# Kernel tuning notes

Measured on AMD Instinct MI355X. Metric: run time of the kernel, lower is better.

## Reference

```python
import jax, jax.numpy as jnp
import numpy as np

CLASS_NUM = 64
CENTROID_MARGIN = 1.4
EPS = 1e-6
N, D = 262144, 128


def setup_inputs() -> dict:
    key = jax.random.key(0)
    k1, k2 = jax.random.split(key)
    embeddings = jax.random.normal(k1, (N, D), dtype=jnp.float32)
    target = jax.random.randint(k2, (N,), 0, CLASS_NUM, dtype=jnp.int32)
    return {"embeddings": embeddings, "target": target}


def reference(embeddings, target):
    C = CLASS_NUM
    dt = embeddings.dtype
    # per-class sums and counts (equivalent to one-hot broadcast-multiply-sum in the original)
    counts = jax.ops.segment_sum(jnp.ones((embeddings.shape[0],), dtype=dt), target, num_segments=C)  # [C]
    sums = jax.ops.segment_sum(embeddings, target, num_segments=C)  # [C, D]
    class_centers = sums / (counts[:, None] + EPS)  # [C, D]
    # pairwise squared distances between centers
    diff = class_centers[:, None, :] - class_centers[None, :, :]  # [C, C, D]
    cc = jnp.sum(diff * diff, axis=2)  # [C, C]
    cc = jax.nn.relu(CENTROID_MARGIN - jnp.sqrt(cc + EPS)) ** 2
    cc = jnp.triu(cc, k=1).sum() / C * (C - 1) / 2
    # L2 distance of each embedding to its class center
    dist = embeddings - class_centers[target]  # [N, D]
    l2 = jnp.sum(dist * dist, axis=1).mean()
    return l2 + cc
```

## Files before the change

### kernel.cpp

```cpp
#include <hip/hip_runtime.h>

#define CLS 64
#define DIM 128
#define NROWS 262144
#define MARGIN 1.4f
#define EPSF 1e-6f
#define FIXSCALE 1048576.0f
#define INVFIX (1.0f / 1048576.0f)
#define NB 512

__global__ __launch_bounds__(512, 2) void phaseA(const float* __restrict__ emb,
                                                 const int* __restrict__ tgt,
                                                 float* __restrict__ psum,
                                                 int* __restrict__ pcnt,
                                                 float* __restrict__ psq,
                                                 int rowsPerBlock) {
    __shared__ int acc[CLS * DIM];
    __shared__ int cnt[CLS];
    __shared__ float red[8];
    const int tid = threadIdx.x;

    for (int i = tid; i < CLS * DIM; i += 512) acc[i] = 0;
    if (tid < CLS) cnt[tid] = 0;
    __syncthreads();

    const int dl = tid & 31;
    const int rl = tid >> 5;
    const int rowBase = blockIdx.x * rowsPerBlock;
    const int iters = rowsPerBlock >> 6;
    int r = rowBase + rl;

    const float4* __restrict__ embv = reinterpret_cast<const float4*>(emb);

    float4 v0 = embv[(size_t)(r)      * 32 + dl];
    float4 v1 = embv[(size_t)(r + 16) * 32 + dl];
    float4 v2 = embv[(size_t)(r + 32) * 32 + dl];
    float4 v3 = embv[(size_t)(r + 48) * 32 + dl];
    int c0 = tgt[r];
    int c1 = tgt[r + 16];
    int c2 = tgt[r + 32];
    int c3 = tgt[r + 48];

    float sq = 0.f;
    for (int it = 0; it < iters; ++it) {
        float4 x0 = v0, x1 = v1, x2 = v2, x3 = v3;
        int k0 = c0, k1 = c1, k2 = c2, k3 = c3;
        int rn = r + 64;
        if (it + 1 < iters) {
            v0 = embv[(size_t)(rn)      * 32 + dl];
            v1 = embv[(size_t)(rn + 16) * 32 + dl];
            v2 = embv[(size_t)(rn + 32) * 32 + dl];
            v3 = embv[(size_t)(rn + 48) * 32 + dl];
            c0 = tgt[rn];
            c1 = tgt[rn + 16];
            c2 = tgt[rn + 32];
            c3 = tgt[rn + 48];
        }
        r = rn;

        sq += x0.x * x0.x + x0.y * x0.y + x0.z * x0.z + x0.w * x0.w;
        sq += x1.x * x1.x + x1.y * x1.y + x1.z * x1.z + x1.w * x1.w;
        sq += x2.x * x2.x + x2.y * x2.y + x2.z * x2.z + x2.w * x2.w;
        sq += x3.x * x3.x + x3.y * x3.y + x3.z * x3.z + x3.w * x3.w;

        int* row0 = &acc[k0 * DIM];
        atomicAdd(&row0[dl],      __float2int_rn(x0.x * FIXSCALE));
        atomicAdd(&row0[32 + dl], __float2int_rn(x0.y * FIXSCALE));
        atomicAdd(&row0[64 + dl], __float2int_rn(x0.z * FIXSCALE));
        atomicAdd(&row0[96 + dl], __float2int_rn(x0.w * FIXSCALE));
        int* row1 = &acc[k1 * DIM];
        atomicAdd(&row1[dl],      __float2int_rn(x1.x * FIXSCALE));
        atomicAdd(&row1[32 + dl], __float2int_rn(x1.y * FIXSCALE));
        atomicAdd(&row1[64 + dl], __float2int_rn(x1.z * FIXSCALE));
        atomicAdd(&row1[96 + dl], __float2int_rn(x1.w * FIXSCALE));
        int* row2 = &acc[k2 * DIM];
        atomicAdd(&row2[dl],      __float2int_rn(x2.x * FIXSCALE));
        atomicAdd(&row2[32 + dl], __float2int_rn(x2.y * FIXSCALE));
        atomicAdd(&row2[64 + dl], __float2int_rn(x2.z * FIXSCALE));
        atomicAdd(&row2[96 + dl], __float2int_rn(x2.w * FIXSCALE));
        int* row3 = &acc[k3 * DIM];
        atomicAdd(&row3[dl],      __float2int_rn(x3.x * FIXSCALE));
        atomicAdd(&row3[32 + dl], __float2int_rn(x3.y * FIXSCALE));
        atomicAdd(&row3[64 + dl], __float2int_rn(x3.z * FIXSCALE));
        atomicAdd(&row3[96 + dl], __float2int_rn(x3.w * FIXSCALE));
        if (dl == 0) {
            atomicAdd(&cnt[k0], 1);
            atomicAdd(&cnt[k1], 1);
            atomicAdd(&cnt[k2], 1);
            atomicAdd(&cnt[k3], 1);
        }
    }

    for (int o = 32; o > 0; o >>= 1) sq += __shfl_down(sq, o, 64);
    if ((tid & 63) == 0) red[tid >> 6] = sq;
    __syncthreads();

    float4* __restrict__ pv = reinterpret_cast<float4*>(psum + (size_t)blockIdx.x * (CLS * DIM));
    const int4* __restrict__ av = reinterpret_cast<const int4*>(acc);
    for (int i = tid; i < (CLS * DIM) / 4; i += 512) {
        int4 a = av[i];
        pv[i] = make_float4((float)a.x * INVFIX, (float)a.y * INVFIX,
                            (float)a.z * INVFIX, (float)a.w * INVFIX);
    }
    if (tid < CLS) pcnt[blockIdx.x * CLS + tid] = cnt[tid];
    if (tid == 0) {
        float s = 0.f;
        for (int k = 0; k < 8; ++k) s += red[k];
        psq[blockIdx.x] = s;
    }
}

__global__ __launch_bounds__(256) void phaseBR(const float* __restrict__ psum,
                                               const int* __restrict__ pcnt,
                                               const float* __restrict__ psq,
                                               float* __restrict__ fsum,
                                               int* __restrict__ fcnt,
                                               double* __restrict__ fsq) {
    const int tid = threadIdx.x;
    if (blockIdx.x < 128) {
        const int o = blockIdx.x * 64 + (tid & 63);
        const int q = tid >> 6;
        const float* __restrict__ p = psum + (size_t)q * 128 * (CLS * DIM) + o;
        float s0 = 0.f, s1 = 0.f, s2 = 0.f, s3 = 0.f;
        for (int j = 0; j < 128; j += 4) {
            s0 += p[(size_t)(j)     * (CLS * DIM)];
            s1 += p[(size_t)(j + 1) * (CLS * DIM)];
            s2 += p[(size_t)(j + 2) * (CLS * DIM)];
            s3 += p[(size_t)(j + 3) * (CLS * DIM)];
        }
        __shared__ float sh[4][64];
        sh[q][tid & 63] = (s0 + s1) + (s2 + s3);
        __syncthreads();
        if (tid < 64) fsum[o] = (sh[0][tid] + sh[1][tid]) + (sh[2][tid] + sh[3][tid]);
    } else {
        const int c = tid & 63;
        const int q = tid >> 6;
        int s = 0;
        for (int k = q * (NB / 4); k < (q + 1) * (NB / 4); ++k) s += pcnt[k * CLS + c];
        __shared__ int shc[4][64];
        shc[q][c] = s;
        __syncthreads();
        if (tid < 64) fcnt[tid] = (shc[0][tid] + shc[1][tid]) + (shc[2][tid] + shc[3][tid]);
        if (tid < 64) {
            double d = 0.0;
            for (int k = tid; k < NB; k += 64) d += (double)psq[k];
            for (int o2 = 32; o2 > 0; o2 >>= 1) d += __shfl_down(d, o2, 64);
            if (tid == 0) fsq[0] = d;
        }
    }
}

__device__ double blockReduceD(double v, double* scratch, int tid) {
    for (int o = 32; o > 0; o >>= 1) v += __shfl_down(v, o, 64);
    if ((tid & 63) == 0) scratch[tid >> 6] = v;
    __syncthreads();
    double t = 0.0;
    if (tid == 0) {
        for (int i = 0; i < 16; ++i) t += scratch[i];
    }
    __syncthreads();
    return t;
}

__global__ __launch_bounds__(1024) void phaseC(const float* __restrict__ fsum,
                                               const int* __restrict__ fcnt,
                                               const double* __restrict__ fsq,
                                               float* __restrict__ out) {
    __shared__ float cenT[DIM][CLS];
    __shared__ float nrm[CLS];
    __shared__ float cInv[CLS];
    __shared__ float cRaw[CLS];
    __shared__ double scratch[16];
    const int tid = threadIdx.x;

    if (tid < CLS) {
        float c = (float)fcnt[tid];
        cRaw[tid] = c;
        cInv[tid] = 1.f / (c + EPSF);
    }
    __syncthreads();

    double s1 = 0.0, s2 = 0.0;
    for (int i = tid; i < CLS * DIM; i += 1024) {
        const int c = i >> 7;
        const int d = i & 127;
        float v = fsum[i];
        float ctr = v * cInv[c];
        cenT[d][c] = ctr;
        s1 += (double)(v * ctr);
        s2 += (double)(cRaw[c] * ctr * ctr);
    }
    const double s1t = blockReduceD(s1, scratch, tid);
    const double s2t = blockReduceD(s2, scratch, tid);

    if (tid < CLS) {
        float n = 0.f;
        for (int d = 0; d < DIM; ++d) {
            float v = cenT[d][tid];
            n += v * v;
        }
        nrm[tid] = n;
    }
    __syncthreads();

    const int w = tid >> 6;
    const int b = tid & 63;
    float g0 = 0.f, g1 = 0.f, g2 = 0.f, g3 = 0.f;
    for (int d = 0; d < DIM; ++d) {
        float vb = cenT[d][b];
        g0 += cenT[d][w]      * vb;
        g1 += cenT[d][w + 16] * vb;
        g2 += cenT[d][w + 32] * vb;
        g3 += cenT[d][w + 48] * vb;
    }
    float ccp = 0.f;
    {
        float gs[4] = {g0, g1, g2, g3};
#pragma unroll
        for (int j = 0; j < 4; ++j) {
            const int a = w + 16 * j;
            if (a == b) continue;
            float d2 = nrm[a] + nrm[b] - 2.f * gs[j];
            float val = fmaxf(MARGIN - sqrtf(fmaxf(d2, 0.f) + EPSF), 0.f);
            ccp += val * val;
        }
    }
    const double ccOrd = blockReduceD((double)ccp, scratch, tid);

    if (tid == 0) {
        double triu = ccOrd * 0.5;
        double ccv = triu / 64.0 * 63.0 / 2.0;
        double l2 = (fsq[0] - 2.0 * s1t + s2t) / (double)NROWS;
        out[0] = (float)(l2 + ccv);
    }
}

extern "C" void kernel_launch(void* const* d_in, const int* in_sizes, int n_in,
                              void* d_out, int out_size, void* d_ws, size_t ws_size,
                              hipStream_t stream) {
    const float* emb = (const float*)d_in[0];
    const int* tgt = (const int*)d_in[1];
    float* out = (float*)d_out;

    char* ws = (char*)d_ws;
    float* fsum = (float*)ws;
    int* fcnt = (int*)(ws + 32768);
    double* fsq = (double*)(ws + 33024);
    float* psum = (float*)(ws + 65536);
    int* pcnt = (int*)(ws + 65536 + (size_t)NB * CLS * DIM * 4);
    float* psq = (float*)(ws + 65536 + (size_t)NB * CLS * DIM * 4 + (size_t)NB * CLS * 4);

    const int rowsPerBlock = NROWS / NB;

    phaseA<<<NB, 512, 0, stream>>>(emb, tgt, psum, pcnt, psq, rowsPerBlock);
    phaseBR<<<129, 256, 0, stream>>>(psum, pcnt, psq, fsum, fcnt, fsq);
    phaseC<<<1, 1024, 0, stream>>>(fsum, fcnt, fsq, out);
}
```

Before: 55.38 us.

## Compute per-class sums via one-hot bf16 MFMA with LDS tree reduction

Replaces shared-memory integer atomics for per-class embedding sums with a one-hot matrix multiply on bf16 MFMA instructions. Each wave accumulates class-by-dim tiles in registers, and the eight waves are combined through a padded LDS tree reduction. Block count is halved and the downstream partial reduction is adjusted to match. It removes LDS atomic contention but truncates embeddings to bf16, which reduces the accuracy of the class centroids.

Measured after the change: 108.6 us. 1.96x slower.

```diff
diff --git a/kernel.cpp b/kernel.cpp
--- a/kernel.cpp
+++ b/kernel.cpp
@@ -5,108 +5,142 @@
 #define NROWS 262144
 #define MARGIN 1.4f
 #define EPSF 1e-6f
-#define FIXSCALE 1048576.0f
-#define INVFIX (1.0f / 1048576.0f)
-#define NB 512
+#define NBLK 256
+#define TPAD 132
+
+typedef __attribute__((ext_vector_type(8))) short bf16x8;
+typedef __attribute__((ext_vector_type(4))) float f32x4;
+
+union BFrag { unsigned u[4]; bf16x8 v; };
+
+__device__ __forceinline__ unsigned pack_bf16(float hi, float lo) {
+    return (__float_as_uint(hi) & 0xFFFF0000u) | (__float_as_uint(lo) >> 16);
+}
 
 __global__ __launch_bounds__(512, 2) void phaseA(const float* __restrict__ emb,
                                                  const int* __restrict__ tgt,
                                                  float* __restrict__ psum,
                                                  int* __restrict__ pcnt,
-                                                 float* __restrict__ psq,
-                                                 int rowsPerBlock) {
-    __shared__ int acc[CLS * DIM];
+                                                 float* __restrict__ psq) {
+    __shared__ float tree[4 * CLS * TPAD];
     __shared__ int cnt[CLS];
-    __shared__ float red[8];
+    __shared__ float lred[8];
+
     const int tid = threadIdx.x;
-
-    for (int i = tid; i < CLS * DIM; i += 512) acc[i] = 0;
+    const int w = tid >> 6;
+    const int l = tid & 63;
+    const int lg = l >> 4;
+    const int li = l & 15;
+
     if (tid < CLS) cnt[tid] = 0;
     __syncthreads();
 
-    const int dl = tid & 31;
-    const int rl = tid >> 5;
-    const int rowBase = blockIdx.x * rowsPerBlock;
-    const int iters = rowsPerBlock >> 6;
-    int r = rowBase + rl;
-
-    const float4* __restrict__ embv = reinterpret_cast<const float4*>(emb);
-
-    float4 v0 = embv[(size_t)(r)      * 32 + dl];
-    float4 v1 = embv[(size_t)(r + 16) * 32 + dl];
-    float4 v2 = embv[(size_t)(r + 32) * 32 + dl];
-    float4 v3 = embv[(size_t)(r + 48) * 32 + dl];
-    int c0 = tgt[r];
-    int c1 = tgt[r + 16];
-    int c2 = tgt[r + 32];
-    int c3 = tgt[r + 48];
+    const int wrow = (blockIdx.x * 8 + w) * 128;
+
+    f32x4 acc[4][8];
+#pragma unroll
+    for (int ct = 0; ct < 4; ++ct)
+#pragma unroll
+        for (int dt = 0; dt < 8; ++dt) {
+            f32x4 z = {0.f, 0.f, 0.f, 0.f};
+            acc[ct][dt] = z;
+        }
 
     float sq = 0.f;
-    for (int it = 0; it < iters; ++it) {
-        float4 x0 = v0, x1 = v1, x2 = v2, x3 = v3;
-        int k0 = c0, k1 = c1, k2 = c2, k3 = c3;
-        int rn = r + 64;
-        if (it + 1 < iters) {
-            v0 = embv[(size_t)(rn)      * 32 + dl];
-            v1 = embv[(size_t)(rn + 16) * 32 + dl];
-            v2 = embv[(size_t)(rn + 32) * 32 + dl];
-            v3 = embv[(size_t)(rn + 48) * 32 + dl];
-            c0 = tgt[rn];
-            c1 = tgt[rn + 16];
-            c2 = tgt[rn + 32];
-            c3 = tgt[rn + 48];
-        }
-        r = rn;
-
-        sq += x0.x * x0.x + x0.y * x0.y + x0.z * x0.z + x0.w * x0.w;
-        sq += x1.x * x1.x + x1.y * x1.y + x1.z * x1.z + x1.w * x1.w;
-        sq += x2.x * x2.x + x2.y * x2.y + x2.z * x2.z + x2.w * x2.w;
-        sq += x3.x * x3.x + x3.y * x3.y + x3.z * x3.z + x3.w * x3.w;
-
-        int* row0 = &acc[k0 * DIM];
-        atomicAdd(&row0[dl],      __float2int_rn(x0.x * FIXSCALE));
-        atomicAdd(&row0[32 + dl], __float2int_rn(x0.y * FIXSCALE));
-        atomicAdd(&row0[64 + dl], __float2int_rn(x0.z * FIXSCALE));
-        atomicAdd(&row0[96 + dl], __float2int_rn(x0.w * FIXSCALE));
-        int* row1 = &acc[k1 * DIM];
-        atomicAdd(&row1[dl],      __float2int_rn(x1.x * FIXSCALE));
-        atomicAdd(&row1[32 + dl], __float2int_rn(x1.y * FIXSCALE));
-        atomicAdd(&row1[64 + dl], __float2int_rn(x1.z * FIXSCALE));
-        atomicAdd(&row1[96 + dl], __float2int_rn(x1.w * FIXSCALE));
-        int* row2 = &acc[k2 * DIM];
-        atomicAdd(&row2[dl],      __float2int_rn(x2.x * FIXSCALE));
-        atomicAdd(&row2[32 + dl], __float2int_rn(x2.y * FIXSCALE));
-        atomicAdd(&row2[64 + dl], __float2int_rn(x2.z * FIXSCALE));
-        atomicAdd(&row2[96 + dl], __float2int_rn(x2.w * FIXSCALE));
-        int* row3 = &acc[k3 * DIM];
-        atomicAdd(&row3[dl],      __float2int_rn(x3.x * FIXSCALE));
-        atomicAdd(&row3[32 + dl], __float2int_rn(x3.y * FIXSCALE));
-        atomicAdd(&row3[64 + dl], __float2int_rn(x3.z * FIXSCALE));
-        atomicAdd(&row3[96 + dl], __float2int_rn(x3.w * FIXSCALE));
-        if (dl == 0) {
-            atomicAdd(&cnt[k0], 1);
-            atomicAdd(&cnt[k1], 1);
-            atomicAdd(&cnt[k2], 1);
-            atomicAdd(&cnt[k3], 1);
+
+#pragma unroll
+    for (int s = 0; s < 4; ++s) {
+        const int rb = wrow + s * 32;
+
+        const int4* tp = reinterpret_cast<const int4*>(tgt + rb + lg * 8);
+        const int4 ta = tp[0];
+        const int4 tb = tp[1];
+
+        if (l < 32) atomicAdd(&cnt[tgt[rb + l]], 1);
+
+        const float* bp = emb + (size_t)(rb + lg * 8) * DIM + li;
+        BFrag B[8];
+#pragma unroll
+        for (int j = 0; j < 4; ++j) {
+            float e0[8], e1[8];
+#pragma unroll
+            for (int dt = 0; dt < 8; ++dt) e0[dt] = bp[(2 * j) * DIM + dt * 16];
+#pragma unroll
+            for (int dt = 0; dt < 8; ++dt) e1[dt] = bp[(2 * j + 1) * DIM + dt * 16];
+#pragma unroll
+            for (int dt = 0; dt < 8; ++dt) {
+                sq += e0[dt] * e0[dt];
+                sq += e1[dt] * e1[dt];
+                B[dt].u[j] = pack_bf16(e1[dt], e0[dt]);
+            }
+        }
+
+        const int tg[8] = {ta.x, ta.y, ta.z, ta.w, tb.x, tb.y, tb.z, tb.w};
+#pragma unroll
+        for (int ct = 0; ct < 4; ++ct) {
+            const int cls = ct * 16 + li;
+            BFrag A;
+#pragma unroll
+            for (int j = 0; j < 4; ++j)
+                A.u[j] = ((tg[2 * j] == cls) ? 0x3F80u : 0u) |
+                         ((tg[2 * j + 1] == cls) ? 0x3F800000u : 0u);
+#pragma unroll
+            for (int dt = 0; dt < 8; ++dt)
+                acc[ct][dt] = __builtin_amdgcn_mfma_f32_16x16x32_bf16(A.v, B[dt].v,
+                                                                      acc[ct][dt], 0, 0, 0);
         }
     }
 
     for (int o = 32; o > 0; o >>= 1) sq += __shfl_down(sq, o, 64);
-    if ((tid & 63) == 0) red[tid >> 6] = sq;
-    __syncthreads();
-
-    float4* __restrict__ pv = reinterpret_cast<float4*>(psum + (size_t)blockIdx.x * (CLS * DIM));
-    const int4* __restrict__ av = reinterpret_cast<const int4*>(acc);
-    for (int i = tid; i < (CLS * DIM) / 4; i += 512) {
-        int4 a = av[i];
-        pv[i] = make_float4((float)a.x * INVFIX, (float)a.y * INVFIX,
-                            (float)a.z * INVFIX, (float)a.w * INVFIX);
+    if (l == 0) lred[w] = sq;
+
+#define TREE_STORE(region)                                                         \
+    {                                                                              \
+        float* dst = &tree[(region) * (CLS * TPAD)];                               \
+        _Pragma("unroll") for (int ct = 0; ct < 4; ++ct)                           \
+            _Pragma("unroll") for (int dt = 0; dt < 8; ++dt)                       \
+                _Pragma("unroll") for (int r = 0; r < 4; ++r)                      \
+                    dst[(ct * 16 + lg * 4 + r) * TPAD + dt * 16 + li] =            \
+                        acc[ct][dt][r];                                            \
+    }
+#define TREE_ADD(region)                                                           \
+    {                                                                              \
+        const float* src = &tree[(region) * (CLS * TPAD)];                         \
+        _Pragma("unroll") for (int ct = 0; ct < 4; ++ct)                           \
+            _Pragma("unroll") for (int dt = 0; dt < 8; ++dt)                       \
+                _Pragma("unroll") for (int r = 0; r < 4; ++r)                      \
+                    acc[ct][dt][r] +=                                              \
+                        src[(ct * 16 + lg * 4 + r) * TPAD + dt * 16 + li];         \
+    }
+
+    __syncthreads();
+    if (w >= 4) TREE_STORE(w - 4);
+    __syncthreads();
+    if (w < 4) TREE_ADD(w);
+    __syncthreads();
+    if (w == 2 || w == 3) TREE_STORE(w - 2);
+    __syncthreads();
+    if (w < 2) TREE_ADD(w);
+    __syncthreads();
+    if (w == 1) TREE_STORE(0);
+    __syncthreads();
+
+    if (w == 0) {
+        TREE_ADD(0);
+        float* __restrict__ ps = psum + (size_t)blockIdx.x * (CLS * DIM);
+#pragma unroll
+        for (int ct = 0; ct < 4; ++ct)
+#pragma unroll
+            for (int dt = 0; dt < 8; ++dt)
+#pragma unroll
+                for (int r = 0; r < 4; ++r)
+                    ps[(ct * 16 + lg * 4 + r) * DIM + dt * 16 + li] = acc[ct][dt][r];
     }
     if (tid < CLS) pcnt[blockIdx.x * CLS + tid] = cnt[tid];
     if (tid == 0) {
-        float s = 0.f;
-        for (int k = 0; k < 8; ++k) s += red[k];
-        psq[blockIdx.x] = s;
+        float t = 0.f;
+        for (int k = 0; k < 8; ++k) t += lred[k];
+        psq[blockIdx.x] = t;
     }
 }
 
@@ -120,9 +154,9 @@
     if (blockIdx.x < 128) {
         const int o = blockIdx.x * 64 + (tid & 63);
         const int q = tid >> 6;
-        const float* __restrict__ p = psum + (size_t)q * 128 * (CLS * DIM) + o;
+        const float* __restrict__ p = psum + (size_t)q * 64 * (CLS * DIM) + o;
         float s0 = 0.f, s1 = 0.f, s2 = 0.f, s3 = 0.f;
-        for (int j = 0; j < 128; j += 4) {
+        for (int j = 0; j < 64; j += 4) {
             s0 += p[(size_t)(j)     * (CLS * DIM)];
             s1 += p[(size_t)(j + 1) * (CLS * DIM)];
             s2 += p[(size_t)(j + 2) * (CLS * DIM)];
@@ -136,14 +170,14 @@
         const int c = tid & 63;
         const int q = tid >> 6;
         int s = 0;
-        for (int k = q * (NB / 4); k < (q + 1) * (NB / 4); ++k) s += pcnt[k * CLS + c];
+        for (int k = q * 64; k < q * 64 + 64; ++k) s += pcnt[k * CLS + c];
         __shared__ int shc[4][64];
         shc[q][c] = s;
         __syncthreads();
         if (tid < 64) fcnt[tid] = (shc[0][tid] + shc[1][tid]) + (shc[2][tid] + shc[3][tid]);
         if (tid < 64) {
             double d = 0.0;
-            for (int k = tid; k < NB; k += 64) d += (double)psq[k];
+            for (int k = tid; k < NBLK; k += 64) d += (double)psq[k];
             for (int o2 = 32; o2 > 0; o2 >>= 1) d += __shfl_down(d, o2, 64);
             if (tid == 0) fsq[0] = d;
         }
@@ -247,12 +281,10 @@
     int* fcnt = (int*)(ws + 32768);
     double* fsq = (double*)(ws + 33024);
     float* psum = (float*)(ws + 65536);
-    int* pcnt = (int*)(ws + 65536 + (size_t)NB * CLS * DIM * 4);
-    float* psq = (float*)(ws + 65536 + (size_t)NB * CLS * DIM * 4 + (size_t)NB * CLS * 4);
-
-    const int rowsPerBlock = NROWS / NB;
-
-    phaseA<<<NB, 512, 0, stream>>>(emb, tgt, psum, pcnt, psq, rowsPerBlock);
+    int* pcnt = (int*)(ws + 65536 + (size_t)NBLK * CLS * DIM * 4);
+    float* psq = (float*)(ws + 65536 + (size_t)NBLK * CLS * DIM * 4 + NBLK * CLS * 4);
+
+    phaseA<<<NBLK, 512, 0, stream>>>(emb, tgt, psum, pcnt, psq);
     phaseBR<<<129, 256, 0, stream>>>(psum, pcnt, psq, fsum, fcnt, fsq);
     phaseC<<<1, 1024, 0, stream>>>(fsum, fcnt, fsq, out);
 }
```
